# Performance work log

Hardware: AMD Instinct MI355X
Metric: run time of the kernel (lower is better)

The kernel has to match this reference:

```python
import jax, jax.numpy as jnp
import numpy as np

N_NODES = 100000
N_EDGES = 1600000
NFEAT, NHID, NCLASS = 512, 128, 16


def gcn_conv(x, edge_index, edge_weight, W, b):
    # Dense linear transform: [N, in] @ [in, out] -> [N, out]
    h = x @ W
    src, dst = edge_index[0], edge_index[1]
    # Edge-weighted gather + scatter-add (message passing)
    msgs = edge_weight[:, None] * h[src]            # [E, out]
    agg = jax.ops.segment_sum(msgs, dst, num_segments=x.shape[0])
    return agg + b


def setup_inputs() -> dict:
    key = jax.random.key(0)
    k = jax.random.split(key, 8)
    x = jax.random.normal(k[0], (N_NODES, NFEAT), dtype=jnp.float32)
    edge_index = jax.random.randint(k[1], (2, N_EDGES), 0, N_NODES, dtype=jnp.int64 if jax.config.jax_enable_x64 else jnp.int32)
    edge_weight = jax.random.uniform(k[2], (N_EDGES,), dtype=jnp.float32)
    # GCNConv glorot-initialized weights + zero biases
    s1 = np.sqrt(6.0 / (NFEAT + NHID)).astype(np.float32)
    s2 = np.sqrt(6.0 / (NHID + NCLASS)).astype(np.float32)
    W1 = jax.random.uniform(k[3], (NFEAT, NHID), minval=-s1, maxval=s1, dtype=jnp.float32)
    b1 = jnp.zeros((NHID,), dtype=jnp.float32)
    W2 = jax.random.uniform(k[4], (NHID, NCLASS), minval=-s2, maxval=s2, dtype=jnp.float32)
    b2 = jnp.zeros((NCLASS,), dtype=jnp.float32)
    return {"x": x, "edge_index": edge_index, "edge_weight": edge_weight,
            "W1": W1, "b1": b1, "W2": W2, "b2": b2}


def reference(x, edge_index, edge_weight, W1, b1, W2, b2):
    # GNNGuard.forward in eval mode (dropout is identity when not training)
    h = jax.nn.relu(gcn_conv(x, edge_index, edge_weight, W1, b1))
    out = gcn_conv(h, edge_index, edge_weight, W2, b2)
    return jax.nn.log_softmax(out, axis=1)
```

## Files before the change

### kernel.cpp

```cpp
#include <hip/hip_runtime.h>
#include <cstdint>
#include <cstddef>


#define NFEAT 512
#define NHID 128
#define NCLASS 16
#define MAXDEG 64
#define Q15 32768.0f
#define IQ15 3.0517578125e-05f

typedef __attribute__((ext_vector_type(8))) __bf16 bf16x8;
typedef __attribute__((ext_vector_type(4))) float f32x4;

__global__ void k_prep_w1(const float* __restrict__ W1, __bf16* __restrict__ W1f) {
    int t = blockIdx.x * 256 + threadIdx.x;
    if (t >= 16 * 8 * 64) return;
    int lane = t & 63;
    int nc = (t >> 6) & 7;
    int ks = t >> 9;
    int q = lane >> 4, col = lane & 15;
    __bf16* outp = W1f + (size_t)t * 8;
#pragma unroll
    for (int j = 0; j < 8; j++) {
        int k = ks * 32 + q * 8 + j;
        int n = nc * 16 + col;
        outp[j] = (__bf16)W1[k * NHID + n];
    }
}

__global__ void k_gemm1_scatter(const float* __restrict__ x, const __bf16* __restrict__ W1f,
                                __bf16* __restrict__ h1b, int M, int nG1,
                                const int* __restrict__ src, const int* __restrict__ dst,
                                const float* __restrict__ ew, int* __restrict__ cnt,
                                uint32_t* __restrict__ pay, int E) {
    if ((int)blockIdx.x >= nG1) {
        int e = (blockIdx.x - nG1) * 256 + threadIdx.x;
        if (e < E) {
            int d = dst[e];
            int r = atomicAdd(&cnt[d], 1);
            if (r < MAXDEG) {
                uint32_t q = (uint32_t)(ew[e] * Q15 + 0.5f);
                if (q > 32767u) q = 32767u;
                pay[(size_t)d * MAXDEG + r] = ((uint32_t)src[e] << 15) | q;
            }
        }
        return;
    }
    int wave = threadIdx.x >> 6;
    int lane = threadIdx.x & 63;
    int q = lane >> 4;
    int col = lane & 15;
    int m0 = blockIdx.x * 64 + wave * 16 + col;
    bool valid = (m0 < M);

    f32x4 acc[8];
#pragma unroll
    for (int n = 0; n < 8; n++) acc[n] = (f32x4)(0.0f);

    const bf16x8* Bf = (const bf16x8*)W1f;
    const float* arow = x + (size_t)m0 * NFEAT + q * 8;

    for (int kk = 0; kk < NFEAT; kk += 32) {
        bf16x8 af;
        if (valid) {
            const f32x4* ap = (const f32x4*)(arow + kk);
            f32x4 a0 = __builtin_nontemporal_load(ap);
            f32x4 a1 = __builtin_nontemporal_load(ap + 1);
            af[0] = (__bf16)a0[0]; af[1] = (__bf16)a0[1];
            af[2] = (__bf16)a0[2]; af[3] = (__bf16)a0[3];
            af[4] = (__bf16)a1[0]; af[5] = (__bf16)a1[1];
            af[6] = (__bf16)a1[2]; af[7] = (__bf16)a1[3];
        } else {
#pragma unroll
            for (int j = 0; j < 8; j++) af[j] = (__bf16)0.0f;
        }
        int kb = (kk >> 5) * 8;
#pragma unroll
        for (int n = 0; n < 8; n++) {
            bf16x8 bf = Bf[(size_t)(kb + n) * 64 + lane];
            acc[n] = __builtin_amdgcn_mfma_f32_16x16x32_bf16(af, bf, acc[n], 0, 0, 0);
        }
    }

    int rbase = blockIdx.x * 64 + wave * 16 + q * 4;
#pragma unroll
    for (int r = 0; r < 4; r++) {
        int row = rbase + r;
        if (row < M) {
            __bf16* op = h1b + (size_t)row * NHID + col;
#pragma unroll
            for (int n = 0; n < 8; n++) op[n * 16] = (__bf16)acc[n][r];
        }
    }
}

__global__ void k_agg1(const uint32_t* __restrict__ h1u, const int* __restrict__ cnt,
                       const uint32_t* __restrict__ pay, const float* __restrict__ b1,
                       uint32_t* __restrict__ hu, int N) {
    int gw = (blockIdx.x * 256 + (int)threadIdx.x) >> 6;
    int lane = threadIdx.x & 63;
    if (gw >= N) return;
    int c = cnt[gw];
    if (c > MAXDEG) c = MAXDEG;
    const uint32_t* prow = pay + (size_t)gw * MAXDEG;
    int sv = 0;
    float wv = 0.f;
    if (lane < c) {
        uint32_t pv = prow[lane];
        sv = (int)(pv >> 15);
        wv = (float)(pv & 32767u) * IQ15;
    }
    float ax = 0.f, ay = 0.f;
    int j = 0;
    for (; j + 8 <= c; j += 8) {
        uint32_t u[8];
        float w[8];
#pragma unroll
        for (int i = 0; i < 8; i++) {
            int s = __shfl(sv, j + i);
            w[i] = __shfl(wv, j + i);
            u[i] = h1u[(size_t)s * 64 + lane];
        }
#pragma unroll
        for (int i = 0; i < 8; i++) {
            ax = fmaf(w[i], __uint_as_float(u[i] << 16), ax);
            ay = fmaf(w[i], __uint_as_float(u[i] & 0xffff0000u), ay);
        }
    }
    for (; j + 4 <= c; j += 4) {
        uint32_t u[4];
        float w[4];
#pragma unroll
        for (int i = 0; i < 4; i++) {
            int s = __shfl(sv, j + i);
            w[i] = __shfl(wv, j + i);
            u[i] = h1u[(size_t)s * 64 + lane];
        }
#pragma unroll
        for (int i = 0; i < 4; i++) {
            ax = fmaf(w[i], __uint_as_float(u[i] << 16), ax);
            ay = fmaf(w[i], __uint_as_float(u[i] & 0xffff0000u), ay);
        }
    }
    for (; j < c; j++) {
        int s = __shfl(sv, j);
        float ww = __shfl(wv, j);
        uint32_t u = h1u[(size_t)s * 64 + lane];
        ax = fmaf(ww, __uint_as_float(u << 16), ax);
        ay = fmaf(ww, __uint_as_float(u & 0xffff0000u), ay);
    }
    float2 bb = ((const float2*)b1)[lane];
    float ox = fmaxf(ax + bb.x, 0.f);
    float oy = fmaxf(ay + bb.y, 0.f);
    union { __bf16 h[2]; uint32_t u; } cvt;
    cvt.h[0] = (__bf16)ox;
    cvt.h[1] = (__bf16)oy;
    hu[(size_t)gw * 64 + lane] = cvt.u;
}

__global__ void k_gemm2(const uint32_t* __restrict__ hu, const float* __restrict__ W2,
                        float* __restrict__ h2, int N) {
    __shared__ float W2s[NHID * NCLASS];
    __shared__ float hs[16][NHID + 4];
    int t = threadIdx.x;
#pragma unroll
    for (int j = 0; j < 8; j++) W2s[t * 8 + j] = W2[t * 8 + j];
    int nb = blockIdx.x * 16;
    {
        int idx = t * 4;
        int row = idx >> 6;
        int kp = idx & 63;
        if (nb + row < N) {
            uint4 u4 = *(const uint4*)(hu + (size_t)(nb + row) * 64 + kp);
            uint32_t us[4] = {u4.x, u4.y, u4.z, u4.w};
#pragma unroll
            for (int j = 0; j < 4; j++) {
                hs[row][(kp + j) * 2 + 0] = __uint_as_float(us[j] << 16);
                hs[row][(kp + j) * 2 + 1] = __uint_as_float(us[j] & 0xffff0000u);
            }
        } else {
#pragma unroll
            for (int j = 0; j < 4; j++) {
                hs[row][(kp + j) * 2 + 0] = 0.f;
                hs[row][(kp + j) * 2 + 1] = 0.f;
            }
        }
    }
    __syncthreads();
    int ni = t >> 4, c = t & 15;
    float acc = 0.f;
#pragma unroll 8
    for (int k = 0; k < NHID; k++) acc = fmaf(hs[ni][k], W2s[k * NCLASS + c], acc);
    if (nb + ni < N) h2[(size_t)(nb + ni) * NCLASS + c] = acc;
}

__global__ void k_agg2(const float* __restrict__ h2, const int* __restrict__ cnt,
                       const uint32_t* __restrict__ pay, const float* __restrict__ b2,
                       float* __restrict__ out, int N) {
    int gw = (blockIdx.x * 256 + (int)threadIdx.x) >> 6;
    int lane = threadIdx.x & 63;
    if (gw >= N) return;
    int c = lane & 15, eg = lane >> 4;
    int n = cnt[gw];
    if (n > MAXDEG) n = MAXDEG;
    const uint32_t* prow = pay + (size_t)gw * MAXDEG;
    int sv = 0;
    float wv = 0.f;
    if (lane < n) {
        uint32_t pv = prow[lane];
        sv = (int)(pv >> 15);
        wv = (float)(pv & 32767u) * IQ15;
    }
    float acc = 0.f;
    int nr = (n + 3) >> 2;
    int i = 0;
    for (; i + 2 <= nr; i += 2) {
        int j0 = i * 4 + eg, j1 = j0 + 4;
        int s0 = __shfl(sv, j0), s1 = __shfl(sv, j1);
        float w0 = __shfl(wv, j0), w1 = __shfl(wv, j1);
        float g0 = h2[(size_t)s0 * NCLASS + c];
        float g1 = h2[(size_t)s1 * NCLASS + c];
        acc = fmaf(w0, g0, acc);
        acc = fmaf(w1, g1, acc);
    }
    if (i < nr) {
        int j0 = i * 4 + eg;
        int s0 = __shfl(sv, j0);
        float w0 = __shfl(wv, j0);
        acc = fmaf(w0, h2[(size_t)s0 * NCLASS + c], acc);
    }
    acc += __shfl_xor(acc, 16);
    acc += __shfl_xor(acc, 32);
    float o = acc + b2[c];
    float m = o;
#pragma unroll
    for (int d = 1; d < 16; d <<= 1) m = fmaxf(m, __shfl_xor(m, d));
    float e = expf(o - m);
    float ssum = e;
#pragma unroll
    for (int d = 1; d < 16; d <<= 1) ssum += __shfl_xor(ssum, d);
    if (lane < 16) out[(size_t)gw * NCLASS + c] = o - m - logf(ssum);
}

extern "C" void kernel_launch(void* const* d_in, const int* in_sizes, int n_in,
                              void* d_out, int out_size, void* d_ws, size_t ws_size,
                              hipStream_t stream) {
    const float* x  = (const float*)d_in[0];
    const int*   ei = (const int*)d_in[1];
    const float* ew = (const float*)d_in[2];
    const float* W1 = (const float*)d_in[3];
    const float* b1 = (const float*)d_in[4];
    const float* W2 = (const float*)d_in[5];
    const float* b2 = (const float*)d_in[6];
    float* out = (float*)d_out;

    int N = in_sizes[0] / NFEAT;
    int E = in_sizes[2];
    const int* srcI = ei;
    const int* dstI = ei + E;

    char* p = (char*)d_ws;
    auto alloc = [&](size_t bytes) {
        char* r = p;
        p += (bytes + 511) & ~(size_t)511;
        return r;
    };
    __bf16*   h1b  = (__bf16*)alloc((size_t)N * NHID * 2);
    uint32_t* hu   = (uint32_t*)alloc((size_t)N * (NHID / 2) * 4);
    float*    h2   = (float*)alloc((size_t)N * NCLASS * 4);
    int*      cnt  = (int*)alloc((size_t)N * 4);
    uint32_t* pay  = (uint32_t*)alloc((size_t)N * MAXDEG * 4);
    __bf16*   W1f  = (__bf16*)alloc((size_t)NFEAT * NHID * 2);

    (void)hipMemsetAsync(cnt, 0, (size_t)N * 4, stream);
    k_prep_w1<<<32, 256, 0, stream>>>(W1, W1f);

    int nG1 = (N + 63) / 64;
    int nSc = (E + 255) / 256;
    k_gemm1_scatter<<<nG1 + nSc, 256, 0, stream>>>(x, W1f, h1b, N, nG1,
                                                   srcI, dstI, ew, cnt, pay, E);

    k_agg1<<<(N + 3) / 4, 256, 0, stream>>>((const uint32_t*)h1b, cnt, pay, b1, hu, N);
    k_gemm2<<<(N + 15) / 16, 256, 0, stream>>>(hu, W2, h2, N);
    k_agg2<<<(N + 3) / 4, 256, 0, stream>>>(h2, cnt, pay, b2, out, N);
}
```

Baseline: 497.9 us.

## Fuse agg1 with gemm2, interleave GEMM/scatter blocks, batch scatter edges

Merges the first aggregation and the second small GEMM into one kernel, so the ReLU'd hidden features stay in shared memory instead of making a global round trip through the hu buffer, and one launch goes away. The combined GEMM1/scatter launch now interleaves GEMM and scatter blocks, and each scatter thread handles four edges with nontemporal loads to overlap the atomic latency. Adds a 4-way unroll to the agg2 gather loop. Each fused block now reloads W2 into LDS for only four nodes, which adds redundant W2 loads.

```diff
diff --git a/kernel.cpp b/kernel.cpp
--- a/kernel.cpp
+++ b/kernel.cpp
@@ -30,28 +30,57 @@
 }
 
 __global__ void k_gemm1_scatter(const float* __restrict__ x, const __bf16* __restrict__ W1f,
-                                __bf16* __restrict__ h1b, int M, int nG1,
+                                __bf16* __restrict__ h1b, int M, int nG1, int nSc,
                                 const int* __restrict__ src, const int* __restrict__ dst,
                                 const float* __restrict__ ew, int* __restrict__ cnt,
                                 uint32_t* __restrict__ pay, int E) {
-    if ((int)blockIdx.x >= nG1) {
-        int e = (blockIdx.x - nG1) * 256 + threadIdx.x;
-        if (e < E) {
-            int d = dst[e];
-            int r = atomicAdd(&cnt[d], 1);
-            if (r < MAXDEG) {
-                uint32_t q = (uint32_t)(ew[e] * Q15 + 0.5f);
-                if (q > 32767u) q = 32767u;
-                pay[(size_t)d * MAXDEG + r] = ((uint32_t)src[e] << 15) | q;
-            }
-        }
+    int bid = blockIdx.x;
+    int nP = nG1 < nSc ? nG1 : nSc;
+    int role, id;
+    if (bid < 2 * nP) { role = bid & 1; id = bid >> 1; }
+    else              { id = bid - nP; role = (nG1 >= nSc) ? 0 : 1; }
+
+    if (role == 1) {
+        int stride = nSc * 256;
+        int base = id * 256 + (int)threadIdx.x;
+        int e0 = base, e1 = base + stride, e2 = base + 2 * stride, e3 = base + 3 * stride;
+        int d0 = 0, d1 = 0, d2 = 0, d3 = 0;
+        int s0 = 0, s1 = 0, s2 = 0, s3 = 0;
+        float w0 = 0.f, w1 = 0.f, w2 = 0.f, w3 = 0.f;
+        bool v0 = e0 < E, v1 = e1 < E, v2 = e2 < E, v3 = e3 < E;
+        if (v0) { d0 = __builtin_nontemporal_load(dst + e0);
+                  s0 = __builtin_nontemporal_load(src + e0);
+                  w0 = __builtin_nontemporal_load(ew + e0); }
+        if (v1) { d1 = __builtin_nontemporal_load(dst + e1);
+                  s1 = __builtin_nontemporal_load(src + e1);
+                  w1 = __builtin_nontemporal_load(ew + e1); }
+        if (v2) { d2 = __builtin_nontemporal_load(dst + e2);
+                  s2 = __builtin_nontemporal_load(src + e2);
+                  w2 = __builtin_nontemporal_load(ew + e2); }
+        if (v3) { d3 = __builtin_nontemporal_load(dst + e3);
+                  s3 = __builtin_nontemporal_load(src + e3);
+                  w3 = __builtin_nontemporal_load(ew + e3); }
+        int r0 = 0, r1 = 0, r2 = 0, r3 = 0;
+        if (v0) r0 = atomicAdd(&cnt[d0], 1);
+        if (v1) r1 = atomicAdd(&cnt[d1], 1);
+        if (v2) r2 = atomicAdd(&cnt[d2], 1);
+        if (v3) r3 = atomicAdd(&cnt[d3], 1);
+        auto pack = [](int s, float w) {
+            uint32_t q = (uint32_t)(w * Q15 + 0.5f);
+            if (q > 32767u) q = 32767u;
+            return ((uint32_t)s << 15) | q;
+        };
+        if (v0 && r0 < MAXDEG) pay[(size_t)d0 * MAXDEG + r0] = pack(s0, w0);
+        if (v1 && r1 < MAXDEG) pay[(size_t)d1 * MAXDEG + r1] = pack(s1, w1);
+        if (v2 && r2 < MAXDEG) pay[(size_t)d2 * MAXDEG + r2] = pack(s2, w2);
+        if (v3 && r3 < MAXDEG) pay[(size_t)d3 * MAXDEG + r3] = pack(s3, w3);
         return;
     }
     int wave = threadIdx.x >> 6;
     int lane = threadIdx.x & 63;
     int q = lane >> 4;
     int col = lane & 15;
-    int m0 = blockIdx.x * 64 + wave * 16 + col;
+    int m0 = id * 64 + wave * 16 + col;
     bool valid = (m0 < M);
 
     f32x4 acc[8];
@@ -83,7 +112,7 @@
         }
     }
 
-    int rbase = blockIdx.x * 64 + wave * 16 + q * 4;
+    int rbase = id * 64 + wave * 16 + q * 4;
 #pragma unroll
     for (int r = 0; r < 4; r++) {
         int row = rbase + r;
@@ -95,104 +124,92 @@
     }
 }
 
-__global__ void k_agg1(const uint32_t* __restrict__ h1u, const int* __restrict__ cnt,
-                       const uint32_t* __restrict__ pay, const float* __restrict__ b1,
-                       uint32_t* __restrict__ hu, int N) {
-    int gw = (blockIdx.x * 256 + (int)threadIdx.x) >> 6;
-    int lane = threadIdx.x & 63;
-    if (gw >= N) return;
-    int c = cnt[gw];
-    if (c > MAXDEG) c = MAXDEG;
-    const uint32_t* prow = pay + (size_t)gw * MAXDEG;
-    int sv = 0;
-    float wv = 0.f;
-    if (lane < c) {
-        uint32_t pv = prow[lane];
-        sv = (int)(pv >> 15);
-        wv = (float)(pv & 32767u) * IQ15;
-    }
-    float ax = 0.f, ay = 0.f;
-    int j = 0;
-    for (; j + 8 <= c; j += 8) {
-        uint32_t u[8];
-        float w[8];
-#pragma unroll
-        for (int i = 0; i < 8; i++) {
-            int s = __shfl(sv, j + i);
-            w[i] = __shfl(wv, j + i);
-            u[i] = h1u[(size_t)s * 64 + lane];
-        }
-#pragma unroll
-        for (int i = 0; i < 8; i++) {
-            ax = fmaf(w[i], __uint_as_float(u[i] << 16), ax);
-            ay = fmaf(w[i], __uint_as_float(u[i] & 0xffff0000u), ay);
-        }
-    }
-    for (; j + 4 <= c; j += 4) {
-        uint32_t u[4];
-        float w[4];
-#pragma unroll
-        for (int i = 0; i < 4; i++) {
-            int s = __shfl(sv, j + i);
-            w[i] = __shfl(wv, j + i);
-            u[i] = h1u[(size_t)s * 64 + lane];
-        }
-#pragma unroll
-        for (int i = 0; i < 4; i++) {
-            ax = fmaf(w[i], __uint_as_float(u[i] << 16), ax);
-            ay = fmaf(w[i], __uint_as_float(u[i] & 0xffff0000u), ay);
-        }
-    }
-    for (; j < c; j++) {
-        int s = __shfl(sv, j);
-        float ww = __shfl(wv, j);
-        uint32_t u = h1u[(size_t)s * 64 + lane];
-        ax = fmaf(ww, __uint_as_float(u << 16), ax);
-        ay = fmaf(ww, __uint_as_float(u & 0xffff0000u), ay);
-    }
-    float2 bb = ((const float2*)b1)[lane];
-    float ox = fmaxf(ax + bb.x, 0.f);
-    float oy = fmaxf(ay + bb.y, 0.f);
-    union { __bf16 h[2]; uint32_t u; } cvt;
-    cvt.h[0] = (__bf16)ox;
-    cvt.h[1] = (__bf16)oy;
-    hu[(size_t)gw * 64 + lane] = cvt.u;
-}
-
-__global__ void k_gemm2(const uint32_t* __restrict__ hu, const float* __restrict__ W2,
-                        float* __restrict__ h2, int N) {
+__global__ void k_agg1g2(const uint32_t* __restrict__ h1u, const int* __restrict__ cnt,
+                         const uint32_t* __restrict__ pay, const float* __restrict__ b1,
+                         const float* __restrict__ W2, float* __restrict__ h2, int N) {
     __shared__ float W2s[NHID * NCLASS];
-    __shared__ float hs[16][NHID + 4];
+    __shared__ float hsf[4][NHID];
     int t = threadIdx.x;
 #pragma unroll
     for (int j = 0; j < 8; j++) W2s[t * 8 + j] = W2[t * 8 + j];
-    int nb = blockIdx.x * 16;
-    {
-        int idx = t * 4;
-        int row = idx >> 6;
-        int kp = idx & 63;
-        if (nb + row < N) {
-            uint4 u4 = *(const uint4*)(hu + (size_t)(nb + row) * 64 + kp);
-            uint32_t us[4] = {u4.x, u4.y, u4.z, u4.w};
-#pragma unroll
-            for (int j = 0; j < 4; j++) {
-                hs[row][(kp + j) * 2 + 0] = __uint_as_float(us[j] << 16);
-                hs[row][(kp + j) * 2 + 1] = __uint_as_float(us[j] & 0xffff0000u);
+
+    int w = t >> 6;
+    int lane = t & 63;
+    int gw = blockIdx.x * 4 + w;
+    bool valid = gw < N;
+
+    float ox = 0.f, oy = 0.f;
+    if (valid) {
+        int c = cnt[gw];
+        if (c > MAXDEG) c = MAXDEG;
+        const uint32_t* prow = pay + (size_t)gw * MAXDEG;
+        int sv = 0;
+        float wv = 0.f;
+        if (lane < c) {
+            uint32_t pv = prow[lane];
+            sv = (int)(pv >> 15);
+            wv = (float)(pv & 32767u) * IQ15;
+        }
+        float ax = 0.f, ay = 0.f;
+        int j = 0;
+        for (; j + 8 <= c; j += 8) {
+            uint32_t u[8];
+            float wgt[8];
+#pragma unroll
+            for (int i = 0; i < 8; i++) {
+                int s = __shfl(sv, j + i);
+                wgt[i] = __shfl(wv, j + i);
+                u[i] = h1u[(size_t)s * 64 + lane];
             }
-        } else {
-#pragma unroll
-            for (int j = 0; j < 4; j++) {
-                hs[row][(kp + j) * 2 + 0] = 0.f;
-                hs[row][(kp + j) * 2 + 1] = 0.f;
+#pragma unroll
+            for (int i = 0; i < 8; i++) {
+                ax = fmaf(wgt[i], __uint_as_float(u[i] << 16), ax);
+                ay = fmaf(wgt[i], __uint_as_float(u[i] & 0xffff0000u), ay);
             }
         }
-    }
+        for (; j + 4 <= c; j += 4) {
+            uint32_t u[4];
+            float wgt[4];
+#pragma unroll
+            for (int i = 0; i < 4; i++) {
+                int s = __shfl(sv, j + i);
+                wgt[i] = __shfl(wv, j + i);
+                u[i] = h1u[(size_t)s * 64 + lane];
+            }
+#pragma unroll
+            for (int i = 0; i < 4; i++) {
+                ax = fmaf(wgt[i], __uint_as_float(u[i] << 16), ax);
+                ay = fmaf(wgt[i], __uint_as_float(u[i] & 0xffff0000u), ay);
+            }
+        }
+        for (; j < c; j++) {
+            int s = __shfl(sv, j);
+            float ww = __shfl(wv, j);
+            uint32_t u = h1u[(size_t)s * 64 + lane];
+            ax = fmaf(ww, __uint_as_float(u << 16), ax);
+            ay = fmaf(ww, __uint_as_float(u & 0xffff0000u), ay);
+        }
+        float2 bb = ((const float2*)b1)[lane];
+        ox = fmaxf(ax + bb.x, 0.f);
+        oy = fmaxf(ay + bb.y, 0.f);
+    }
+    hsf[w][2 * lane + 0] = ox;
+    hsf[w][2 * lane + 1] = oy;
     __syncthreads();
-    int ni = t >> 4, c = t & 15;
+
+    int node = t >> 6;
+    int c16 = (t >> 2) & 15;
+    int q4 = t & 3;
     float acc = 0.f;
-#pragma unroll 8
-    for (int k = 0; k < NHID; k++) acc = fmaf(hs[ni][k], W2s[k * NCLASS + c], acc);
-    if (nb + ni < N) h2[(size_t)(nb + ni) * NCLASS + c] = acc;
+#pragma unroll
+    for (int j = 0; j < 32; j++) {
+        int k = q4 + j * 4;
+        acc = fmaf(hsf[node][k], W2s[k * NCLASS + c16], acc);
+    }
+    acc += __shfl_down(acc, 1);
+    acc += __shfl_down(acc, 2);
+    int gn = blockIdx.x * 4 + node;
+    if (q4 == 0 && gn < N) h2[(size_t)gn * NCLASS + c16] = acc;
 }
 
 __global__ void k_agg2(const float* __restrict__ h2, const int* __restrict__ cnt,
@@ -215,6 +232,21 @@
     float acc = 0.f;
     int nr = (n + 3) >> 2;
     int i = 0;
+    for (; i + 4 <= nr; i += 4) {
+        int j0 = i * 4 + eg;
+        int s0 = __shfl(sv, j0), s1 = __shfl(sv, j0 + 4);
+        int s2 = __shfl(sv, j0 + 8), s3 = __shfl(sv, j0 + 12);
+        float w0 = __shfl(wv, j0), w1 = __shfl(wv, j0 + 4);
+        float w2 = __shfl(wv, j0 + 8), w3 = __shfl(wv, j0 + 12);
+        float g0 = h2[(size_t)s0 * NCLASS + c];
+        float g1 = h2[(size_t)s1 * NCLASS + c];
+        float g2 = h2[(size_t)s2 * NCLASS + c];
+        float g3 = h2[(size_t)s3 * NCLASS + c];
+        acc = fmaf(w0, g0, acc);
+        acc = fmaf(w1, g1, acc);
+        acc = fmaf(w2, g2, acc);
+        acc = fmaf(w3, g3, acc);
+    }
     for (; i + 2 <= nr; i += 2) {
         int j0 = i * 4 + eg, j1 = j0 + 4;
         int s0 = __shfl(sv, j0), s1 = __shfl(sv, j1);
@@ -267,7 +299,6 @@
         return r;
     };
     __bf16*   h1b  = (__bf16*)alloc((size_t)N * NHID * 2);
-    uint32_t* hu   = (uint32_t*)alloc((size_t)N * (NHID / 2) * 4);
     float*    h2   = (float*)alloc((size_t)N * NCLASS * 4);
     int*      cnt  = (int*)alloc((size_t)N * 4);
     uint32_t* pay  = (uint32_t*)alloc((size_t)N * MAXDEG * 4);
@@ -277,11 +308,10 @@
     k_prep_w1<<<32, 256, 0, stream>>>(W1, W1f);
 
     int nG1 = (N + 63) / 64;
-    int nSc = (E + 255) / 256;
-    k_gemm1_scatter<<<nG1 + nSc, 256, 0, stream>>>(x, W1f, h1b, N, nG1,
+    int nSc = (E + 1023) / 1024;
+    k_gemm1_scatter<<<nG1 + nSc, 256, 0, stream>>>(x, W1f, h1b, N, nG1, nSc,
                                                    srcI, dstI, ew, cnt, pay, E);
 
-    k_agg1<<<(N + 3) / 4, 256, 0, stream>>>((const uint32_t*)h1b, cnt, pay, b1, hu, N);
-    k_gemm2<<<(N + 15) / 16, 256, 0, stream>>>(hu, W2, h2, N);
+    k_agg1g2<<<(N + 3) / 4, 256, 0, stream>>>((const uint32_t*)h1b, cnt, pay, b1, W2, h2, N);
     k_agg2<<<(N + 3) / 4, 256, 0, stream>>>(h2, cnt, pay, b2, out, N);
 }
```

Result: slower. 546.0 us (+9.7%).
